# Kernel optimization log

Hardware: AMD Instinct MI355X
Metric: run time of the kernel (lower is better)

## Reference

```python
import jax, jax.numpy as jnp
import numpy as np

EMBED = 1024
HEAD = 64


def setup_inputs() -> dict:
    key = jax.random.key(0)
    kx, kq, kk, kv = jax.random.split(key, 4)
    x = jax.random.normal(kx, (8, 2048, EMBED), dtype=jnp.float32)
    s = EMBED ** -0.5  # init scale for weights
    Wq = jax.random.normal(kq, (EMBED, HEAD), dtype=jnp.float32) * s
    Wk = jax.random.normal(kk, (EMBED, HEAD), dtype=jnp.float32) * s
    Wv = jax.random.normal(kv, (EMBED, HEAD), dtype=jnp.float32) * s
    return {"x": x, "Wq": Wq, "Wk": Wk, "Wv": Wv}


def reference(x, Wq, Wk, Wv):
    # x: [B, T, C]; single-head causal attention, scale = C**-0.5 (embed dim, as in source)
    B, T, C = x.shape
    q = jnp.einsum('btc,ch->bth', x, Wq)
    k = jnp.einsum('btc,ch->bth', x, Wk)
    v = jnp.einsum('btc,ch->bth', x, Wv)
    w = jnp.einsum('bqh,bkh->bqk', q, k) * (C ** -0.5)  # [B, T, T]
    causal = jnp.tril(jnp.ones((T, T), dtype=bool))
    w = jnp.where(causal, w, -jnp.inf)
    w = jax.nn.softmax(w, axis=-1)
    # dropout = 0.0 (eval-mode reference) -> identity
    return jnp.einsum('bqk,bkh->bqh', w, v)  # [B, T, head]
```

## Files before the change

kernel.cpp:

```cpp
#include <hip/hip_runtime.h>
#include <stdint.h>

typedef unsigned short u16;
typedef __attribute__((ext_vector_type(8))) short short8;
typedef __attribute__((ext_vector_type(4))) float f32x4;
typedef __attribute__((ext_vector_type(16))) float f32x16;

#define B_ 8
#define T_ 2048
#define C_ 1024
#define D_ 64
#define PSC 0.04508422f

__device__ inline u16 f2bf(float f) {
  union { float f; uint32_t u; } v; v.f = f;
  uint32_t u = v.u;
  return (u16)((u + 0x7fffu + ((u >> 16) & 1u)) >> 16);
}
__device__ inline uint32_t pack2(float lo, float hi) {
  return (uint32_t)f2bf(lo) | ((uint32_t)f2bf(hi) << 16);
}

__global__ __launch_bounds__(256) void wt_kernel(const float* __restrict__ Wq,
                                                 const float* __restrict__ Wk,
                                                 const float* __restrict__ Wv,
                                                 u16* __restrict__ wfrag) {
  const int mi = blockIdx.x >> 4;
  const int k0 = (blockIdx.x & 15) * 64;
  const float* W = (mi == 0) ? Wq : ((mi == 1) ? Wk : Wv);
  __shared__ u16 tr[64 * 68];

  const int t = threadIdx.x;
  {
    const int n = t & 63, kr0 = (t >> 6) * 16;
#pragma unroll
    for (int j = 0; j < 16; ++j)
      tr[n * 68 + kr0 + j] = f2bf(W[(size_t)(k0 + kr0 + j) * 64 + n]);
  }
  __syncthreads();
  {
    const int n = t >> 2, q16 = (t & 3) * 16;
    const int n16g = mi * 4 + (n >> 4);
#pragma unroll
    for (int h = 0; h < 2; ++h) {
      const int kr = q16 + h * 8;
      const int kchunk = (k0 + kr) >> 5;
      const int lane = (n & 15) + 16 * ((kr >> 3) & 3);
      uint32_t pk[4];
#pragma unroll
      for (int jj = 0; jj < 4; ++jj)
        pk[jj] = (uint32_t)tr[n * 68 + kr + 2 * jj] | ((uint32_t)tr[n * 68 + kr + 2 * jj + 1] << 16);
      *(uint4*)&wfrag[(((size_t)n16g * 32 + kchunk) * 64 + lane) * 8] = *(uint4*)&pk[0];
    }
  }
}

__global__ __launch_bounds__(256, 2) void qkv_kernel(const float* __restrict__ x,
                                                     const u16* __restrict__ wfrag,
                                                     u16* __restrict__ qfr,
                                                     u16* __restrict__ kfr,
                                                     u16* __restrict__ vfr) {
  __shared__ __align__(16) u16 xl[2][32 * 64];

  const int tid = threadIdx.x;
  const int ng = tid >> 6, l = tid & 63;
  const int lo16 = l & 15, hi4 = l >> 4;
  const int m0 = blockIdx.x * 32;

  const int xrow = tid >> 3;
  const int xc8 = tid & 7;
  const float* xs0 = x + (size_t)(m0 + xrow) * C_ + xc8 * 8;
  u16* xdst0 = &xl[0][xrow * 64 + ((xc8 ^ (xrow & 7)) << 3)];
  u16* xdst1 = &xl[1][xrow * 64 + ((xc8 ^ (xrow & 7)) << 3)];

  f32x4 acc[2][3];
#pragma unroll
  for (int rf = 0; rf < 2; ++rf)
#pragma unroll
    for (int j = 0; j < 3; ++j) acc[rf][j] = {0.f, 0.f, 0.f, 0.f};

  const u16* wbase = wfrag + (size_t)(ng * 3) * 32 * 512 + l * 8;
  short8 wA[6], wB[6];
  float4 xf0, xf1;

  {
    float4 f0 = *(const float4*)(xs0 + 0);
    float4 f1 = *(const float4*)(xs0 + 4);
    uint32_t p[4] = {pack2(f0.x, f0.y), pack2(f0.z, f0.w), pack2(f1.x, f1.y), pack2(f1.z, f1.w)};
    *(uint4*)xdst0 = *(uint4*)&p[0];
#pragma unroll
    for (int i = 0; i < 6; ++i)
      wA[i] = *(const short8*)(wbase + ((i >> 1) * 32 + (i & 1)) * 512);
  }
  __syncthreads();

#define QKV_STEP(KT, XR, XW, WC, WN)                                          \
  {                                                                           \
    if ((KT) < 15) {                                                          \
      const float* xs = xs0 + ((KT) + 1) * 64;                                \
      xf0 = *(const float4*)(xs + 0);                                         \
      xf1 = *(const float4*)(xs + 4);                                         \
      _Pragma("unroll")                                                       \
      for (int i = 0; i < 6; ++i)                                             \
        WN[i] = *(const short8*)(wbase + ((i >> 1) * 32 + ((KT) + 1) * 2 + (i & 1)) * 512); \
    }                                                                         \
    _Pragma("unroll")                                                         \
    for (int k32 = 0; k32 < 2; ++k32) {                                       \
      const int ac = k32 * 4 + hi4;                                           \
      _Pragma("unroll")                                                       \
      for (int rf = 0; rf < 2; ++rf) {                                        \
        const int arow = rf * 16 + lo16;                                      \
        short8 a = *(const short8*)&XR[arow * 64 + ((ac ^ (arow & 7)) << 3)]; \
        _Pragma("unroll")                                                     \
        for (int j = 0; j < 3; ++j)                                           \
          acc[rf][j] = __builtin_amdgcn_mfma_f32_16x16x32_bf16(a, WC[j * 2 + k32], acc[rf][j], 0, 0, 0); \
      }                                                                       \
    }                                                                         \
    if ((KT) < 15) {                                                          \
      uint32_t p[4] = {pack2(xf0.x, xf0.y), pack2(xf0.z, xf0.w),              \
                       pack2(xf1.x, xf1.y), pack2(xf1.z, xf1.w)};             \
      *(uint4*)XW = *(uint4*)&p[0];                                           \
    }                                                                         \
    __syncthreads();                                                          \
  }

#pragma unroll 1
  for (int kt = 0; kt < 16; kt += 2) {
    QKV_STEP(kt, xl[0], xdst1, wA, wB)
    QKV_STEP(kt + 1, xl[1], xdst0, wB, wA)
  }
#undef QKV_STEP

  const int bb = m0 >> 11;
  const int tok_b = m0 & 2047;
#pragma unroll
  for (int rf = 0; rf < 2; ++rf) {
    const int row0 = rf * 16 + hi4 * 4;
    const int tok0 = tok_b + row0;
    const int tt = tok0 >> 6;
    const int t32 = tok0 >> 5;
#pragma unroll
    for (int j = 0; j < 3; ++j) {
      const int cb = ng * 48 + j * 16;
      const int mt = cb >> 6;
      const int col = (cb & 63) + lo16;
      if (mt == 0) {
        const int cs = col >> 4;
        const int lane0 = (tok0 & 31) + 32 * ((col >> 3) & 1);
        u16* qp = qfr + ((((size_t)bb * 64 + t32) * 4 + cs) * 64 + lane0) * 8 + (col & 7);
#pragma unroll
        for (int r = 0; r < 4; ++r) qp[(size_t)r * 8] = f2bf(acc[rf][j][r] * PSC);
      } else if (mt == 1) {
        const int h = (tok0 >> 5) & 1;
        const int cs = col >> 4;
        const int lane0 = (tok0 & 31) + 32 * ((col >> 3) & 1);
        u16* kp = kfr + (((((size_t)bb * 32 + tt) * 2 + h) * 4 + cs) * 64 + lane0) * 8 + (col & 7);
#pragma unroll
        for (int r = 0; r < 4; ++r) kp[(size_t)r * 8] = f2bf(acc[rf][j][r]);
      } else {
        const int ks = (tok0 >> 4) & 3;
        const int hi = (tok0 >> 3) & 1;
        const int jj = tok0 & 7;
        const int lane = (col & 31) + 32 * hi;
        const int df = col >> 5;
        uint2 st = {pack2(acc[rf][j][0], acc[rf][j][1]), pack2(acc[rf][j][2], acc[rf][j][3])};
        *(uint2*)&vfr[((((((size_t)bb * 32 + tt) * 4 + ks) * 2 + df) * 64 + lane) * 8 + jj)] = st;
      }
    }
  }
}

__global__ __launch_bounds__(256, 2) void attn_kernel(const u16* __restrict__ qfr,
                                                      const u16* __restrict__ kfr,
                                                      const u16* __restrict__ vfr,
                                                      float* __restrict__ out) {
  __shared__ float o_lds[4][32][68];
  __shared__ float l_lds[4][64];

  const int tid = threadIdx.x;
  const int w = tid >> 6, l = tid & 63;
  const int l31 = l & 31, hi1 = l >> 5;
  const int b = blockIdx.x;
  const int y = blockIdx.y;
  const int qt = (y < 32) ? (63 - 2 * y) : (2 * (y - 32));
  const int qbase = qt * 32;
  const int boff = b * T_;
  const int NT = (qt + 2) >> 1;

  short8 qf[4];
  {
    const u16* qp = qfr + (size_t)(b * 64 + qt) * 4 * 512 + l * 8;
#pragma unroll
    for (int cs = 0; cs < 4; ++cs) qf[cs] = *(const short8*)(qp + cs * 512);
  }

  const u16* kfb = kfr + (size_t)b * 32 * 4096 + l * 8;
  const u16* vfb = vfr + (size_t)b * 32 * 4096 + l * 8;

  f32x16 O0, O1;
#pragma unroll
  for (int r = 0; r < 16; ++r) { O0[r] = 0.f; O1[r] = 0.f; }
  float lsum = 0.f;

  short8 kf[2][4];
#define LOADK(T) { const u16* kp = kfb + (size_t)(T) * 4096; \
  _Pragma("unroll") for (int h2 = 0; h2 < 2; ++h2) \
  _Pragma("unroll") for (int cs = 0; cs < 4; ++cs) \
    kf[h2][cs] = *(const short8*)(kp + (h2 * 4 + cs) * 512); }

  if (w < NT) LOADK(w);

  union { uint32_t u[4]; short8 v; } pu;
  short8 pa[4];

  for (int t = w; t < NT; t += 4) {
    const int k0 = t * 64;

    f32x16 s0, s1;
#pragma unroll
    for (int r = 0; r < 16; ++r) { s0[r] = 0.f; s1[r] = 0.f; }
    __builtin_amdgcn_s_setprio(1);
#pragma unroll
    for (int cs = 0; cs < 4; ++cs) {
      s0 = __builtin_amdgcn_mfma_f32_32x32x16_bf16(kf[0][cs], qf[cs], s0, 0, 0, 0);
      s1 = __builtin_amdgcn_mfma_f32_32x32x16_bf16(kf[1][cs], qf[cs], s1, 0, 0, 0);
    }
    __builtin_amdgcn_s_setprio(0);

    short8 vf[4][2];
    {
      const u16* vp = vfb + (size_t)t * 4096;
#pragma unroll
      for (int ks = 0; ks < 4; ++ks)
#pragma unroll
        for (int df = 0; df < 2; ++df)
          vf[ks][df] = *(const short8*)(vp + (ks * 2 + df) * 512);
    }

    if (t + 4 < NT) LOADK(t + 4);

    if (k0 + 63 > qbase) {
#pragma unroll
      for (int r = 0; r < 16; ++r) {
        const int kr = (r & 3) + 8 * (r >> 2) + 4 * hi1;
        if (k0 + kr > qbase + l31) s0[r] = -1e30f;
        if (k0 + 32 + kr > qbase + l31) s1[r] = -1e30f;
      }
    }

    float p0[16], p1[16];
    float ts[4] = {0.f, 0.f, 0.f, 0.f};
#pragma unroll
    for (int r = 0; r < 16; ++r) {
      p0[r] = exp2f(s0[r]);
      p1[r] = exp2f(s1[r]);
      ts[r & 3] += p0[r] + p1[r];
    }
    lsum += (ts[0] + ts[1]) + (ts[2] + ts[3]);

#define REDIST(KS, ARR) { \
    const int s8 = ((KS) & 1) * 8; \
    uint32_t c0a = pack2(ARR[s8 + 0], ARR[s8 + 1]); \
    uint32_t c0b = pack2(ARR[s8 + 2], ARR[s8 + 3]); \
    uint32_t c1a = pack2(ARR[s8 + 4], ARR[s8 + 5]); \
    uint32_t c1b = pack2(ARR[s8 + 6], ARR[s8 + 7]); \
    uint32_t fa = hi1 ? c0a : c1a; \
    uint32_t fb = hi1 ? c0b : c1b; \
    uint32_t ga = __shfl_xor(fa, 32); \
    uint32_t gb = __shfl_xor(fb, 32); \
    pu.u[0] = hi1 ? ga : c0a; \
    pu.u[1] = hi1 ? gb : c0b; \
    pu.u[2] = hi1 ? c1a : ga; \
    pu.u[3] = hi1 ? c1b : gb; \
    pa[KS] = pu.v; }
    REDIST(0, p0)
    REDIST(1, p0)
    REDIST(2, p1)
    REDIST(3, p1)
#undef REDIST

    __builtin_amdgcn_s_setprio(1);
#pragma unroll
    for (int ks = 0; ks < 4; ++ks) {
      O0 = __builtin_amdgcn_mfma_f32_32x32x16_bf16(pa[ks], vf[ks][0], O0, 0, 0, 0);
      O1 = __builtin_amdgcn_mfma_f32_32x32x16_bf16(pa[ks], vf[ks][1], O1, 0, 0, 0);
    }
    __builtin_amdgcn_s_setprio(0);
  }
#undef LOADK

#pragma unroll
  for (int r = 0; r < 16; ++r) {
    const int qr = (r & 3) + 8 * (r >> 2) + 4 * hi1;
    o_lds[w][qr][l31] = O0[r];
    o_lds[w][qr][32 + l31] = O1[r];
  }
  l_lds[w][l] = lsum;
  __syncthreads();

  {
    const int q = tid >> 3;
    const int d8 = (tid & 7) * 8;
    float lacc = 0.f;
    float oacc[8] = {0.f, 0.f, 0.f, 0.f, 0.f, 0.f, 0.f, 0.f};
#pragma unroll
    for (int s = 0; s < 4; ++s) {
      lacc += l_lds[s][q] + l_lds[s][q + 32];
#pragma unroll
      for (int j = 0; j < 8; ++j) oacc[j] += o_lds[s][q][d8 + j];
    }
    const float inv = 1.f / lacc;
    float4 r0 = {oacc[0] * inv, oacc[1] * inv, oacc[2] * inv, oacc[3] * inv};
    float4 r1 = {oacc[4] * inv, oacc[5] * inv, oacc[6] * inv, oacc[7] * inv};
    float* op = out + (size_t)(boff + qbase + q) * 64 + d8;
    *(float4*)(op + 0) = r0;
    *(float4*)(op + 4) = r1;
  }
}

extern "C" void kernel_launch(void* const* d_in, const int* in_sizes, int n_in,
                              void* d_out, int out_size, void* d_ws, size_t ws_size,
                              hipStream_t stream) {
  const float* x  = (const float*)d_in[0];
  const float* Wq = (const float*)d_in[1];
  const float* Wk = (const float*)d_in[2];
  const float* Wv = (const float*)d_in[3];
  float* out = (float*)d_out;

  u16* ws    = (u16*)d_ws;
  u16* wfrag = ws;
  u16* qfr   = ws + 196608;
  u16* kfr   = qfr + 1048576;
  u16* vfr   = kfr + 1048576;

  wt_kernel<<<dim3(48), dim3(256), 0, stream>>>(Wq, Wk, Wv, wfrag);
  qkv_kernel<<<dim3(512), dim3(256), 0, stream>>>(x, wfrag, qfr, kfr, vfr);
  attn_kernel<<<dim3(8, 64), dim3(256), 0, stream>>>(qfr, kfr, vfr, out);
}
```

Before: 40.84 us.

## Deepen QKV x-prefetch pipeline and split QK MFMA accumulation chains

The QKV projection loop now prefetches x rows two k-tiles ahead in registers instead of one and is restructured with a peeled tail, so global load latency has more MFMA work to hide behind. In the attention loop the V fragment loads are issued before the QK^T MFMAs. The QK^T reduction is split into two independent accumulator chains that are summed afterwards, which breaks the MFMA dependency chain. The main loop is also marked unroll 1. The costs are higher register pressure and extra vector adds, which could lower occupancy.

```diff
diff --git a/kernel.cpp b/kernel.cpp
--- a/kernel.cpp
+++ b/kernel.cpp
@@ -81,55 +81,65 @@
 
   const u16* wbase = wfrag + (size_t)(ng * 3) * 32 * 512 + l * 8;
   short8 wA[6], wB[6];
-  float4 xf0, xf1;
+  float4 xr1a, xr1b, xr2a, xr2b;
+
+#define LOADW(DST, KT)                                                        \
+  _Pragma("unroll")                                                           \
+  for (int i = 0; i < 6; ++i)                                                 \
+    DST[i] = *(const short8*)(wbase + ((i >> 1) * 32 + (KT) * 2 + (i & 1)) * 512);
+
+#define PACKX(A0, A1, DST)                                                    \
+  { uint32_t p[4] = {pack2(A0.x, A0.y), pack2(A0.z, A0.w),                    \
+                     pack2(A1.x, A1.y), pack2(A1.z, A1.w)};                   \
+    *(uint4*)DST = *(uint4*)&p[0]; }
+
+#define MFMA6(XR, WC)                                                         \
+  _Pragma("unroll")                                                           \
+  for (int k32 = 0; k32 < 2; ++k32) {                                         \
+    const int ac = k32 * 4 + hi4;                                             \
+    _Pragma("unroll")                                                         \
+    for (int rf = 0; rf < 2; ++rf) {                                          \
+      const int arow = rf * 16 + lo16;                                        \
+      short8 a = *(const short8*)&XR[arow * 64 + ((ac ^ (arow & 7)) << 3)];   \
+      _Pragma("unroll")                                                       \
+      for (int j = 0; j < 3; ++j)                                             \
+        acc[rf][j] = __builtin_amdgcn_mfma_f32_16x16x32_bf16(a, WC[j * 2 + k32], acc[rf][j], 0, 0, 0); \
+    }                                                                         \
+  }
 
   {
     float4 f0 = *(const float4*)(xs0 + 0);
     float4 f1 = *(const float4*)(xs0 + 4);
-    uint32_t p[4] = {pack2(f0.x, f0.y), pack2(f0.z, f0.w), pack2(f1.x, f1.y), pack2(f1.z, f1.w)};
-    *(uint4*)xdst0 = *(uint4*)&p[0];
-#pragma unroll
-    for (int i = 0; i < 6; ++i)
-      wA[i] = *(const short8*)(wbase + ((i >> 1) * 32 + (i & 1)) * 512);
+    PACKX(f0, f1, xdst0)
+    xr1a = *(const float4*)(xs0 + 64);
+    xr1b = *(const float4*)(xs0 + 68);
+    LOADW(wA, 0)
   }
   __syncthreads();
 
-#define QKV_STEP(KT, XR, XW, WC, WN)                                          \
-  {                                                                           \
-    if ((KT) < 15) {                                                          \
-      const float* xs = xs0 + ((KT) + 1) * 64;                                \
-      xf0 = *(const float4*)(xs + 0);                                         \
-      xf1 = *(const float4*)(xs + 4);                                         \
-      _Pragma("unroll")                                                       \
-      for (int i = 0; i < 6; ++i)                                             \
-        WN[i] = *(const short8*)(wbase + ((i >> 1) * 32 + ((KT) + 1) * 2 + (i & 1)) * 512); \
-    }                                                                         \
-    _Pragma("unroll")                                                         \
-    for (int k32 = 0; k32 < 2; ++k32) {                                       \
-      const int ac = k32 * 4 + hi4;                                           \
-      _Pragma("unroll")                                                       \
-      for (int rf = 0; rf < 2; ++rf) {                                        \
-        const int arow = rf * 16 + lo16;                                      \
-        short8 a = *(const short8*)&XR[arow * 64 + ((ac ^ (arow & 7)) << 3)]; \
-        _Pragma("unroll")                                                     \
-        for (int j = 0; j < 3; ++j)                                           \
-          acc[rf][j] = __builtin_amdgcn_mfma_f32_16x16x32_bf16(a, WC[j * 2 + k32], acc[rf][j], 0, 0, 0); \
-      }                                                                       \
-    }                                                                         \
-    if ((KT) < 15) {                                                          \
-      uint32_t p[4] = {pack2(xf0.x, xf0.y), pack2(xf0.z, xf0.w),              \
-                       pack2(xf1.x, xf1.y), pack2(xf1.z, xf1.w)};             \
-      *(uint4*)XW = *(uint4*)&p[0];                                           \
-    }                                                                         \
-    __syncthreads();                                                          \
-  }
-
 #pragma unroll 1
-  for (int kt = 0; kt < 16; kt += 2) {
-    QKV_STEP(kt, xl[0], xdst1, wA, wB)
-    QKV_STEP(kt + 1, xl[1], xdst0, wB, wA)
-  }
-#undef QKV_STEP
+  for (int kt = 0; kt < 14; kt += 2) {
+    xr2a = *(const float4*)(xs0 + (kt + 2) * 64);
+    xr2b = *(const float4*)(xs0 + (kt + 2) * 64 + 4);
+    LOADW(wB, kt + 1)
+    MFMA6(xl[0], wA)
+    PACKX(xr1a, xr1b, xdst1)
+    __syncthreads();
+    xr1a = *(const float4*)(xs0 + (kt + 3) * 64);
+    xr1b = *(const float4*)(xs0 + (kt + 3) * 64 + 4);
+    LOADW(wA, kt + 2)
+    MFMA6(xl[1], wB)
+    PACKX(xr2a, xr2b, xdst0)
+    __syncthreads();
+  }
+  LOADW(wB, 15)
+  MFMA6(xl[0], wA)
+  PACKX(xr1a, xr1b, xdst1)
+  __syncthreads();
+  MFMA6(xl[1], wB)
+#undef LOADW
+#undef PACKX
+#undef MFMA6
 
   const int bb = m0 >> 11;
   const int tok_b = m0 & 2047;
@@ -213,19 +223,9 @@
   union { uint32_t u[4]; short8 v; } pu;
   short8 pa[4];
 
+#pragma unroll 1
   for (int t = w; t < NT; t += 4) {
     const int k0 = t * 64;
-
-    f32x16 s0, s1;
-#pragma unroll
-    for (int r = 0; r < 16; ++r) { s0[r] = 0.f; s1[r] = 0.f; }
-    __builtin_amdgcn_s_setprio(1);
-#pragma unroll
-    for (int cs = 0; cs < 4; ++cs) {
-      s0 = __builtin_amdgcn_mfma_f32_32x32x16_bf16(kf[0][cs], qf[cs], s0, 0, 0, 0);
-      s1 = __builtin_amdgcn_mfma_f32_32x32x16_bf16(kf[1][cs], qf[cs], s1, 0, 0, 0);
-    }
-    __builtin_amdgcn_s_setprio(0);
 
     short8 vf[4][2];
     {
@@ -236,6 +236,21 @@
         for (int df = 0; df < 2; ++df)
           vf[ks][df] = *(const short8*)(vp + (ks * 2 + df) * 512);
     }
+
+    f32x16 s0, s1, s0b, s1b;
+#pragma unroll
+    for (int r = 0; r < 16; ++r) { s0[r] = 0.f; s1[r] = 0.f; s0b[r] = 0.f; s1b[r] = 0.f; }
+    __builtin_amdgcn_s_setprio(1);
+#pragma unroll
+    for (int cs = 0; cs < 2; ++cs) {
+      s0 = __builtin_amdgcn_mfma_f32_32x32x16_bf16(kf[0][cs], qf[cs], s0, 0, 0, 0);
+      s1 = __builtin_amdgcn_mfma_f32_32x32x16_bf16(kf[1][cs], qf[cs], s1, 0, 0, 0);
+      s0b = __builtin_amdgcn_mfma_f32_32x32x16_bf16(kf[0][cs + 2], qf[cs + 2], s0b, 0, 0, 0);
+      s1b = __builtin_amdgcn_mfma_f32_32x32x16_bf16(kf[1][cs + 2], qf[cs + 2], s1b, 0, 0, 0);
+    }
+    __builtin_amdgcn_s_setprio(0);
+#pragma unroll
+    for (int r = 0; r < 16; ++r) { s0[r] += s0b[r]; s1[r] += s1b[r]; }
 
     if (t + 4 < NT) LOADK(t + 4);
 
```

Result: faster. 38.68 us (-5.3%).
